# Kernel optimization log

Measured on AMD Instinct MI355X. Metric: run time of the kernel, lower is better.

The kernel has to match this reference:

```python
import jax, jax.numpy as jnp
import numpy as np

D_MODEL = 768
NUM_HEADS = 12
DEPTH = D_MODEL // NUM_HEADS
LN_EPS = 1e-5


def setup_inputs() -> dict:
    key = jax.random.key(0)
    ks = jax.random.split(key, 5)
    B, S = 2, 2048
    scale = 1.0 / np.sqrt(D_MODEL)
    return {
        "Q": jax.random.normal(ks[0], (B, S, D_MODEL), jnp.float32),
        "W_q": jax.random.normal(ks[1], (D_MODEL, D_MODEL), jnp.float32) * scale,
        "b_q": jnp.zeros((D_MODEL,), jnp.float32),
        "W_k": jax.random.normal(ks[2], (D_MODEL, D_MODEL), jnp.float32) * scale,
        "b_k": jnp.zeros((D_MODEL,), jnp.float32),
        "W_v": jax.random.normal(ks[3], (D_MODEL, D_MODEL), jnp.float32) * scale,
        "b_v": jnp.zeros((D_MODEL,), jnp.float32),
        "W_o": jax.random.normal(ks[4], (D_MODEL, D_MODEL), jnp.float32) * scale,
        "b_o": jnp.zeros((D_MODEL,), jnp.float32),
        "ln_gamma": jnp.ones((D_MODEL,), jnp.float32),
        "ln_beta": jnp.zeros((D_MODEL,), jnp.float32),
    }


def _split_heads(x, B):
    # [B, S, D] -> [B, H, S, depth]
    return x.reshape(B, -1, NUM_HEADS, DEPTH).transpose(0, 2, 1, 3)


def reference(Q, W_q, b_q, W_k, b_k, W_v, b_v, W_o, b_o, ln_gamma, ln_beta):
    B = Q.shape[0]
    residual = Q
    # torch Linear: x @ W.T + b
    q = _split_heads(Q @ W_q.T + b_q, B)  # [B,H,S,dh]
    k = _split_heads(Q @ W_k.T + b_k, B)
    v = _split_heads(Q @ W_v.T + b_v, B)
    scores = jnp.einsum("bhqd,bhkd->bhqk", q, k) / jnp.sqrt(jnp.float32(DEPTH))
    attn = jax.nn.softmax(scores, axis=-1)
    out = jnp.einsum("bhqk,bhkd->bhqd", attn, v)
    out = out.transpose(0, 2, 1, 3).reshape(B, -1, D_MODEL)
    out = out @ W_o.T + b_o
    x = out + residual
    mu = jnp.mean(x, axis=-1, keepdims=True)
    var = jnp.mean(jnp.square(x - mu), axis=-1, keepdims=True)
    return (x - mu) * jax.lax.rsqrt(var + LN_EPS) * ln_gamma + ln_beta
```

## Files before the change

kernel.cpp:

```cpp
#include <hip/hip_runtime.h>
#include <hip/hip_bf16.h>

#define D_MODEL 768
#define S_LEN   2048
#define BATCH   2
#define NHEAD   12
#define DH      64
#define NTOK    (BATCH * S_LEN)
#define NBH     (BATCH * NHEAD)

typedef __attribute__((ext_vector_type(8))) short bf16x8;
typedef __attribute__((ext_vector_type(4))) float f32x4;

__device__ inline unsigned short f2bf(float f) {
    union { float f; unsigned u; } v; v.f = f;
    unsigned u = v.u;
    u += 0x7fffu + ((u >> 16) & 1u);
    return (unsigned short)(u >> 16);
}

__device__ inline unsigned pack_bf2(float a, float b) {
    union { __hip_bfloat162 h2; unsigned u; } cv;
    cv.h2 = __float22bfloat162_rn(make_float2(a, b));
    return cv.u;
}

__device__ inline float bf2f(unsigned short u) {
    union { unsigned u; float f; } c; c.u = ((unsigned)u) << 16; return c.f;
}

__device__ inline void stage16(const void* g, void* l) {
    __builtin_amdgcn_global_load_lds(
        (const __attribute__((address_space(1))) unsigned*)g,
        (__attribute__((address_space(3))) unsigned*)l, 16, 0, 0);
}

__global__ __launch_bounds__(256) void convert_kernel(
    const float* __restrict__ Q,
    const float* __restrict__ Wq, const float* __restrict__ Wk,
    const float* __restrict__ Wv, const float* __restrict__ Wo,
    unsigned short* __restrict__ Xb,
    unsigned short* __restrict__ Wqb, unsigned short* __restrict__ Wkb,
    unsigned short* __restrict__ Wvb, unsigned short* __restrict__ Wob)
{
    const int XV = NTOK * D_MODEL / 4;
    const int WV = D_MODEL * D_MODEL / 4;
    int idx = blockIdx.x * 256 + threadIdx.x;
    if (idx >= XV + 4 * WV) return;

    const float* src; unsigned short* dst; int off;
    if (idx < XV) { src = Q; dst = Xb; off = idx; }
    else {
        int i2 = idx - XV;
        int seg = i2 / WV; off = i2 - seg * WV;
        if      (seg == 0) { src = Wq; dst = Wqb; }
        else if (seg == 1) { src = Wk; dst = Wkb; }
        else if (seg == 2) { src = Wv; dst = Wvb; }
        else               { src = Wo; dst = Wob; }
    }
    float4 v = reinterpret_cast<const float4*>(src)[off];
    uint2 o;
    o.x = pack_bf2(v.x, v.y);
    o.y = pack_bf2(v.z, v.w);
    reinterpret_cast<uint2*>(dst)[off] = o;
}

#define STAGE_TILE(glob, rowstrideB, row0, k0, ldsbase, nIss)                 \
    _Pragma("unroll")                                                          \
    for (int i = 0; i < (nIss); ++i) {                                         \
        int L = i * 4096 + wv * 1024 + lane * 16;                              \
        int row = L >> 7;                                                      \
        int colb = (L & 127) ^ ((row & 7) << 4);                               \
        stage16((const char*)(glob) + (size_t)((row0) + row) * (rowstrideB)    \
                    + ((k0) << 1) + colb,                                      \
                (char*)(ldsbase) + i * 4096 + wv * 1024);                      \
    }

__global__ __launch_bounds__(256) void qkv_gemm_kernel(
    const unsigned short* __restrict__ Xb,
    const unsigned short* __restrict__ Wall,
    const float* __restrict__ bq, const float* __restrict__ bk,
    const float* __restrict__ bv,
    unsigned short* __restrict__ qb, unsigned short* __restrict__ kb,
    unsigned short* __restrict__ vtb)
{
    const int lane = threadIdx.x & 63;
    const int wv   = threadIdx.x >> 6;
    const int lr   = lane & 15;
    const int lg   = lane >> 4;
    const int row0g = blockIdx.y * 128;
    const int col0g = blockIdx.x * 64;

    __shared__ __align__(16) unsigned short At[2][128 * 64];
    __shared__ __align__(16) unsigned short Bt[2][64 * 64];

    f32x4 acc[2][4] = {};

    STAGE_TILE(Xb,   1536, row0g, 0, At[0], 4);
    STAGE_TILE(Wall, 1536, col0g, 0, Bt[0], 2);
    __syncthreads();

    for (int s = 0; s < 12; ++s) {
        int cur = s & 1;
        if (s < 11) {
            STAGE_TILE(Xb,   1536, row0g, (s + 1) * 64, At[cur ^ 1], 4);
            STAGE_TILE(Wall, 1536, col0g, (s + 1) * 64, Bt[cur ^ 1], 2);
        }
        bf16x8 a[2][2], b[4][2];
#pragma unroll
        for (int m = 0; m < 2; ++m) {
            int row = wv * 32 + m * 16 + lr, sw = (row & 7) << 4;
#pragma unroll
            for (int ks = 0; ks < 2; ++ks)
                a[m][ks] = *reinterpret_cast<const bf16x8*>(
                    (const char*)At[cur] + row * 128 + ((ks * 64 + lg * 16) ^ sw));
        }
#pragma unroll
        for (int n = 0; n < 4; ++n) {
            int row = n * 16 + lr, sw = (row & 7) << 4;
#pragma unroll
            for (int ks = 0; ks < 2; ++ks)
                b[n][ks] = *reinterpret_cast<const bf16x8*>(
                    (const char*)Bt[cur] + row * 128 + ((ks * 64 + lg * 16) ^ sw));
        }
#pragma unroll
        for (int ks = 0; ks < 2; ++ks)
#pragma unroll
            for (int m = 0; m < 2; ++m)
#pragma unroll
                for (int n = 0; n < 4; ++n)
                    acc[m][n] = __builtin_amdgcn_mfma_f32_16x16x32_bf16(
                        a[m][ks], b[n][ks], acc[m][n], 0, 0, 0);
        __syncthreads();
    }

    const int which   = blockIdx.x / 12;
    const int colbase = (blockIdx.x % 12) * 64;
    const float* bias = (which == 0) ? bq : (which == 1) ? bk : bv;
#pragma unroll
    for (int m = 0; m < 2; ++m) {
#pragma unroll
        for (int n = 0; n < 4; ++n) {
            int col = colbase + n * 16 + lr;
            float bval = bias[col];
            int h = col >> 6, d = col & 63;
            int rowg = row0g + wv * 32 + m * 16 + lg * 4;
            int bb = rowg >> 11, s0 = rowg & 2047;
            if (which == 2) {
                uint2 w;
                w.x = pack_bf2(acc[m][n][0] + bval, acc[m][n][1] + bval);
                w.y = pack_bf2(acc[m][n][2] + bval, acc[m][n][3] + bval);
                *reinterpret_cast<uint2*>(
                    vtb + ((size_t)(bb * NHEAD + h) * DH + d) * S_LEN + s0) = w;
            } else {
                unsigned short* dst = (which == 0) ? qb : kb;
#pragma unroll
                for (int r = 0; r < 4; ++r)
                    dst[((size_t)(bb * NHEAD + h) * S_LEN + s0 + r) * DH + d] =
                        f2bf(acc[m][n][r] + bval);
            }
        }
    }
}

#define ATTN_CHUNK(P, CI, NCHUNK)                                              \
    {                                                                          \
        if ((CI) < (NCHUNK) - 1) {                                             \
            _Pragma("unroll")                                                  \
            for (int i = 0; i < SPW; ++i) {                                    \
                stage16(kg[i], sdK[(P) ^ 1] + i * 1024);                       \
                stage16(vg[i], sdV[(P) ^ 1] + i * 1024);                       \
                kg[i] += 8192; vg[i] += 128;                                   \
            }                                                                  \
        }                                                                      \
        f32x4 s[4] = {};                                                       \
        __builtin_amdgcn_s_setprio(1);                                         \
        _Pragma("unroll")                                                      \
        for (int kt = 0; kt < 4; ++kt) {                                       \
            bf16x8 ak0 = *(const bf16x8*)(rdK[P] + kt * 2048);                 \
            bf16x8 ak1 = *(const bf16x8*)(rdK[P] + kt * 2048 + oD);            \
            s[kt] = __builtin_amdgcn_mfma_f32_16x16x32_bf16(ak0, bq0, s[kt], 0, 0, 0); \
            s[kt] = __builtin_amdgcn_mfma_f32_16x16x32_bf16(ak1, bq1, s[kt], 0, 0, 0); \
        }                                                                      \
        __builtin_amdgcn_s_setprio(0);                                         \
        bf16x8 av0[4], av1[4];                                                 \
        _Pragma("unroll")                                                      \
        for (int t = 0; t < 4; ++t) {                                          \
            av0[t] = *(const bf16x8*)(rdV[P] + t * 2048);                      \
            av1[t] = *(const bf16x8*)(rdV[P] + t * 2048 + oD);                 \
        }                                                                      \
        float mxr = fmaxf(fmaxf(fmaxf(s[0][0], s[0][1]), fmaxf(s[0][2], s[0][3])), \
                          fmaxf(fmaxf(s[1][0], s[1][1]), fmaxf(s[1][2], s[1][3]))); \
        mxr = fmaxf(mxr, fmaxf(fmaxf(fmaxf(s[2][0], s[2][1]), fmaxf(s[2][2], s[2][3])), \
                               fmaxf(fmaxf(s[3][0], s[3][1]), fmaxf(s[3][2], s[3][3])))); \
        mxr = fmaxf(mxr, __shfl_xor(mxr, 16));                                 \
        mxr = fmaxf(mxr, __shfl_xor(mxr, 32));                                 \
        float mxs = mxr * SC;                                                  \
        if (__any(mxs > m + 8.0f)) {                                           \
            float mn = fmaxf(m, mxs);                                          \
            float sf = __builtin_amdgcn_exp2f(m - mn);                         \
            m = mn; l *= sf;                                                   \
            _Pragma("unroll")                                                  \
            for (int t = 0; t < 4; ++t) acc[t] *= sf;                          \
        }                                                                      \
        float p[16];                                                           \
        _Pragma("unroll")                                                      \
        for (int kt = 0; kt < 4; ++kt)                                         \
            _Pragma("unroll")                                                  \
            for (int r = 0; r < 4; ++r)                                        \
                p[kt * 4 + r] = __builtin_amdgcn_exp2f(fmaf(s[kt][r], SC, -m)); \
        float sum = ((p[0] + p[1]) + (p[2] + p[3])) + ((p[4] + p[5]) + (p[6] + p[7])); \
        sum += ((p[8] + p[9]) + (p[10] + p[11])) + ((p[12] + p[13]) + (p[14] + p[15])); \
        sum += __shfl_xor(sum, 16);                                            \
        sum += __shfl_xor(sum, 32);                                            \
        l += sum;                                                              \
        _Pragma("unroll")                                                      \
        for (int kt = 0; kt < 4; ++kt) {                                       \
            uint2 w;                                                           \
            w.x = pack_bf2(p[kt * 4 + 0], p[kt * 4 + 1]);                      \
            w.y = pack_bf2(p[kt * 4 + 2], p[kt * 4 + 3]);                      \
            *(uint2*)(plw + kt * 32 + lg * 8) = w;                             \
        }                                                                      \
        union { bf16x8 v; uint2 u[2]; } bp0, bp1;                              \
        bp0.u[0] = *(const uint2*)(plr);                                       \
        bp0.u[1] = *(const uint2*)(plr + 8);                                   \
        bp1.u[0] = *(const uint2*)(plr + 64);                                  \
        bp1.u[1] = *(const uint2*)(plr + 72);                                  \
        __builtin_amdgcn_s_setprio(1);                                         \
        _Pragma("unroll")                                                      \
        for (int t = 0; t < 4; ++t) {                                          \
            acc[t] = __builtin_amdgcn_mfma_f32_16x16x32_bf16(av0[t], bp0.v, acc[t], 0, 0, 0); \
            acc[t] = __builtin_amdgcn_mfma_f32_16x16x32_bf16(av1[t], bp1.v, acc[t], 0, 0, 0); \
        }                                                                      \
        __builtin_amdgcn_s_setprio(0);                                         \
        __syncthreads();                                                       \
    }

template<int NW, int KS>
__global__ __launch_bounds__(NW * 64) void attn_kernel(
    const unsigned short* __restrict__ qb, const unsigned short* __restrict__ kb,
    const unsigned short* __restrict__ vtb,
    unsigned short* __restrict__ attnb,
    unsigned short* __restrict__ Opart,
    float2* __restrict__ mlbuf)
{
    constexpr int SPW    = 8192 / (NW * 1024);
    constexpr int NCHUNK = 32 / KS;

    const int lane = threadIdx.x & 63;
    const int wv   = threadIdx.x >> 6;
    const int lr   = lane & 15;
    const int lg   = lane >> 4;
    const int bh   = blockIdx.y;
    const int h    = bh % NHEAD, bb = bh / NHEAD;
    const int q0   = blockIdx.x * (NW * 16) + wv * 16;
    const int ks   = (KS == 2) ? blockIdx.z : 0;

    __shared__ __align__(16) unsigned short Kt[2][4096];
    __shared__ __align__(16) unsigned short Vt[2][4096];
    __shared__ __align__(16) unsigned short PL[NW][16][68];

    const char* kbase = (const char*)(kb  + (size_t)bh * S_LEN * DH)
                        + (size_t)ks * (S_LEN / KS) * 128;
    const char* vbase = (const char*)(vtb + (size_t)bh * DH * S_LEN)
                        + (size_t)ks * (S_LEN / KS) * 2;
    const unsigned short* qptr = qb + ((size_t)bh * S_LEN + q0) * DH;

    bf16x8 bq0 = *reinterpret_cast<const bf16x8*>(qptr + (size_t)lr * DH + lg * 8);
    bf16x8 bq1 = *reinterpret_cast<const bf16x8*>(qptr + (size_t)lr * DH + 32 + lg * 8);

    const int swr = (lr & 7) << 4;
    const int o0  = (lg * 16) ^ swr;
    const int oD  = (o0 ^ 64) - o0;

    const char* kg[SPW];
    const char* vg[SPW];
#pragma unroll
    for (int i = 0; i < SPW; ++i) {
        int L = wv * SPW * 1024 + i * 1024 + lane * 16;
        int r = L >> 7;
        int c = (L & 127) ^ ((r & 7) << 4);
        kg[i] = kbase + (size_t)r * 128 + c;
        vg[i] = vbase + (size_t)r * 4096 + c;
    }
    char* sdK[2] = { (char*)Kt[0] + wv * SPW * 1024, (char*)Kt[1] + wv * SPW * 1024 };
    char* sdV[2] = { (char*)Vt[0] + wv * SPW * 1024, (char*)Vt[1] + wv * SPW * 1024 };
    const char* rdK[2] = {
        (const char*)Kt[0] + lr * 128 + o0,
        (const char*)Kt[1] + lr * 128 + o0 };
    const char* rdV[2] = {
        (const char*)Vt[0] + lr * 128 + o0,
        (const char*)Vt[1] + lr * 128 + o0 };
    char* plw = (char*)PL + wv * 2176 + lr * 136;
    const char* plr = plw + lg * 16;

    float m = -1e30f, l = 0.f;
    f32x4 acc[4] = {};
    const float SC = 0.125f * 1.44269504088896f;

#pragma unroll
    for (int i = 0; i < SPW; ++i) {
        stage16(kg[i], sdK[0] + i * 1024);
        stage16(vg[i], sdV[0] + i * 1024);
        kg[i] += 8192; vg[i] += 128;
    }
    __syncthreads();

    for (int it = 0; it < NCHUNK / 2; ++it) {
        ATTN_CHUNK(0, it * 2, NCHUNK);
        ATTN_CHUNK(1, it * 2 + 1, NCHUNK);
    }

    if constexpr (KS == 1) {
        float rl = 1.0f / l;
        size_t rowbase = ((size_t)(bb * S_LEN + q0 + lr)) * D_MODEL + h * DH;
#pragma unroll
        for (int t = 0; t < 4; ++t) {
            unsigned w0 = pack_bf2(acc[t][0] * rl, acc[t][1] * rl);
            unsigned w1 = pack_bf2(acc[t][2] * rl, acc[t][3] * rl);
            *reinterpret_cast<unsigned*>(attnb + rowbase + t * 16 + lg * 4)     = w0;
            *reinterpret_cast<unsigned*>(attnb + rowbase + t * 16 + lg * 4 + 2) = w1;
        }
    } else {
        size_t base = ((size_t)(ks * NBH + bh) * S_LEN + q0 + lr) * 64;
#pragma unroll
        for (int t = 0; t < 4; ++t) {
            unsigned w0 = pack_bf2(acc[t][0], acc[t][1]);
            unsigned w1 = pack_bf2(acc[t][2], acc[t][3]);
            *reinterpret_cast<unsigned*>(Opart + base + t * 16 + lg * 4)     = w0;
            *reinterpret_cast<unsigned*>(Opart + base + t * 16 + lg * 4 + 2) = w1;
        }
        if (lg == 0)
            mlbuf[(size_t)(ks * NBH + bh) * S_LEN + q0 + lr] = make_float2(m, l);
    }
}

__global__ __launch_bounds__(256) void combine_kernel(
    const unsigned short* __restrict__ Opart,
    const float2* __restrict__ mlbuf,
    unsigned short* __restrict__ attnb)
{
    int idx = blockIdx.x * 256 + threadIdx.x;
    int d4  = idx & 15;
    int h   = (idx >> 4) % 12;
    int tok = idx / 192;
    int bb  = tok >> 11, s = tok & 2047;
    size_t qoff = (size_t)(bb * NHEAD + h) * S_LEN + s;

    float2 ml0 = mlbuf[qoff];
    float2 ml1 = mlbuf[(size_t)NBH * S_LEN + qoff];
    float M  = fmaxf(ml0.x, ml1.x);
    float w0 = __builtin_amdgcn_exp2f(ml0.x - M);
    float w1 = __builtin_amdgcn_exp2f(ml1.x - M);
    float ri = 1.0f / (w0 * ml0.y + w1 * ml1.y);
    w0 *= ri; w1 *= ri;

    size_t ob = qoff * 64 + d4 * 4;
    ushort4 a = *reinterpret_cast<const ushort4*>(Opart + ob);
    ushort4 b = *reinterpret_cast<const ushort4*>(Opart + (size_t)NBH * S_LEN * 64 + ob);
    float o0 = bf2f(a.x) * w0 + bf2f(b.x) * w1;
    float o1 = bf2f(a.y) * w0 + bf2f(b.y) * w1;
    float o2 = bf2f(a.z) * w0 + bf2f(b.z) * w1;
    float o3 = bf2f(a.w) * w0 + bf2f(b.w) * w1;
    uint2 w;
    w.x = pack_bf2(o0, o1);
    w.y = pack_bf2(o2, o3);
    *reinterpret_cast<uint2*>(attnb + (size_t)tok * D_MODEL + h * 64 + d4 * 4) = w;
}

__global__ __launch_bounds__(256) void oproj_kernel(
    const unsigned short* __restrict__ attnb, const unsigned short* __restrict__ Wob,
    const float* __restrict__ bo, const float* __restrict__ Qres,
    float* __restrict__ Y)
{
    const int lane = threadIdx.x & 63;
    const int wv   = threadIdx.x >> 6;
    const int lr   = lane & 15;
    const int lg   = lane >> 4;
    const int row0g = blockIdx.y * 128;
    const int col0g = blockIdx.x * 64;

    __shared__ __align__(16) unsigned short At[2][128 * 64];
    __shared__ __align__(16) unsigned short Bt[2][64 * 64];

    f32x4 acc[2][4] = {};

    STAGE_TILE(attnb, 1536, row0g, 0, At[0], 4);
    STAGE_TILE(Wob,   1536, col0g, 0, Bt[0], 2);
    __syncthreads();

    for (int s = 0; s < 12; ++s) {
        int cur = s & 1;
        if (s < 11) {
            STAGE_TILE(attnb, 1536, row0g, (s + 1) * 64, At[cur ^ 1], 4);
            STAGE_TILE(Wob,   1536, col0g, (s + 1) * 64, Bt[cur ^ 1], 2);
        }
        bf16x8 a[2][2], b[4][2];
#pragma unroll
        for (int m = 0; m < 2; ++m) {
            int row = wv * 32 + m * 16 + lr, sw = (row & 7) << 4;
#pragma unroll
            for (int ks = 0; ks < 2; ++ks)
                a[m][ks] = *reinterpret_cast<const bf16x8*>(
                    (const char*)At[cur] + row * 128 + ((ks * 64 + lg * 16) ^ sw));
        }
#pragma unroll
        for (int n = 0; n < 4; ++n) {
            int row = n * 16 + lr, sw = (row & 7) << 4;
#pragma unroll
            for (int ks = 0; ks < 2; ++ks)
                b[n][ks] = *reinterpret_cast<const bf16x8*>(
                    (const char*)Bt[cur] + row * 128 + ((ks * 64 + lg * 16) ^ sw));
        }
#pragma unroll
        for (int ks = 0; ks < 2; ++ks)
#pragma unroll
            for (int m = 0; m < 2; ++m)
#pragma unroll
                for (int n = 0; n < 4; ++n)
                    acc[m][n] = __builtin_amdgcn_mfma_f32_16x16x32_bf16(
                        a[m][ks], b[n][ks], acc[m][n], 0, 0, 0);
        __syncthreads();
    }

#pragma unroll
    for (int m = 0; m < 2; ++m)
#pragma unroll
        for (int n = 0; n < 4; ++n) {
            int col = col0g + n * 16 + lr;
            float bval = bo[col];
#pragma unroll
            for (int r = 0; r < 4; ++r) {
                int row = row0g + wv * 32 + m * 16 + lg * 4 + r;
                size_t off = (size_t)row * D_MODEL + col;
                Y[off] = acc[m][n][r] + bval + Qres[off];
            }
        }
}

__global__ __launch_bounds__(256) void ln_kernel(
    const float* __restrict__ Y,
    const float* __restrict__ gamma, const float* __restrict__ beta,
    float* __restrict__ out)
{
    const int lane = threadIdx.x & 63;
    const int row  = blockIdx.x * 4 + (threadIdx.x >> 6);
    const float4* yr = reinterpret_cast<const float4*>(Y + (size_t)row * D_MODEL);

    float4 v[3];
    float sum = 0.f, ss = 0.f;
#pragma unroll
    for (int j = 0; j < 3; ++j) {
        v[j] = yr[lane + 64 * j];
        sum += v[j].x + v[j].y + v[j].z + v[j].w;
        ss  += v[j].x * v[j].x + v[j].y * v[j].y + v[j].z * v[j].z + v[j].w * v[j].w;
    }
#pragma unroll
    for (int msk = 1; msk < 64; msk <<= 1) {
        sum += __shfl_xor(sum, msk);
        ss  += __shfl_xor(ss,  msk);
    }
    float mu  = sum * (1.f / 768.f);
    float var = ss * (1.f / 768.f) - mu * mu;
    float is  = rsqrtf(var + 1e-5f);

    const float4* g4 = reinterpret_cast<const float4*>(gamma);
    const float4* b4 = reinterpret_cast<const float4*>(beta);
    float4* o4 = reinterpret_cast<float4*>(out + (size_t)row * D_MODEL);
#pragma unroll
    for (int j = 0; j < 3; ++j) {
        float4 g = g4[lane + 64 * j], b = b4[lane + 64 * j], r;
        r.x = (v[j].x - mu) * is * g.x + b.x;
        r.y = (v[j].y - mu) * is * g.y + b.y;
        r.z = (v[j].z - mu) * is * g.z + b.z;
        r.w = (v[j].w - mu) * is * g.w + b.w;
        o4[lane + 64 * j] = r;
    }
}

extern "C" void kernel_launch(void* const* d_in, const int* in_sizes, int n_in,
                              void* d_out, int out_size, void* d_ws, size_t ws_size,
                              hipStream_t stream)
{
    const float* Q     = (const float*)d_in[0];
    const float* Wq    = (const float*)d_in[1];
    const float* bq    = (const float*)d_in[2];
    const float* Wk    = (const float*)d_in[3];
    const float* bk    = (const float*)d_in[4];
    const float* Wv    = (const float*)d_in[5];
    const float* bv    = (const float*)d_in[6];
    const float* Wo    = (const float*)d_in[7];
    const float* bo    = (const float*)d_in[8];
    const float* gamma = (const float*)d_in[9];
    const float* beta  = (const float*)d_in[10];
    float* out = (float*)d_out;

    char* ws = (char*)d_ws;
    unsigned short* Xb    = (unsigned short*)(ws + 0);
    unsigned short* Wqb   = (unsigned short*)(ws + 6291456);
    unsigned short* Wkb   = (unsigned short*)(ws + 7471104);
    unsigned short* Wvb   = (unsigned short*)(ws + 8650752);
    unsigned short* Wob   = (unsigned short*)(ws + 9830400);
    unsigned short* qb    = (unsigned short*)(ws + 11010048);
    unsigned short* kb    = (unsigned short*)(ws + 17301504);
    unsigned short* vtb   = (unsigned short*)(ws + 23592960);
    unsigned short* attnb = (unsigned short*)(ws + 29884416);
    float*          Yf    = (float*)        (ws + 36175872);
    unsigned short* Opartb = (unsigned short*)(ws + 36175872);
    float2*         mlbuf  = (float2*)       (ws + 61341696);

    const bool splitk = (ws_size >= 62128128ull);

    convert_kernel<<<5376, 256, 0, stream>>>(Q, Wq, Wk, Wv, Wo, Xb, Wqb, Wkb, Wvb, Wob);
    qkv_gemm_kernel<<<dim3(36, 32), 256, 0, stream>>>(Xb, Wqb, bq, bk, bv, qb, kb, vtb);
    if (splitk) {
        attn_kernel<8, 2><<<dim3(16, 24, 2), 512, 0, stream>>>(qb, kb, vtb, attnb,
                                                               Opartb, mlbuf);
        combine_kernel<<<3072, 256, 0, stream>>>(Opartb, mlbuf, attnb);
    } else {
        attn_kernel<4, 1><<<dim3(32, 24), 256, 0, stream>>>(qb, kb, vtb, attnb,
                                                            Opartb, mlbuf);
    }
    oproj_kernel<<<dim3(12, 32), 256, 0, stream>>>(attnb, Wob, bo, Q, Yf);
    ln_kernel<<<1024, 256, 0, stream>>>(Yf, gamma, beta, out);
}
```

Baseline: 111.4 us.

## Triple-buffer K in attention, read V directly from global, enlarge QKV GEMM tiles

The QKV GEMM tile goes from 128x64 to 128x128, with a 2x2 warp layout and four by four accumulators per warp, so each block reuses its X tile across twice as many output columns. The attention kernel now triple-buffers only K in LDS, using explicit vmcnt waits and raw barriers instead of __syncthreads. V fragments are loaded straight from global memory per lane, and the cross-lane sum reductions and the max shuffles are deferred or moved inside the rare rescale branch. The non-split path moves to 512-thread blocks. This aims to cut LDS traffic, barrier stalls and shuffle work, at the cost of uncoalesced direct V global loads and more register pressure in the GEMM.

```diff
diff --git a/kernel.cpp b/kernel.cpp
--- a/kernel.cpp
+++ b/kernel.cpp
@@ -88,36 +88,38 @@
     const int wv   = threadIdx.x >> 6;
     const int lr   = lane & 15;
     const int lg   = lane >> 4;
+    const int wr   = wv >> 1;
+    const int wc   = wv & 1;
     const int row0g = blockIdx.y * 128;
-    const int col0g = blockIdx.x * 64;
+    const int col0g = blockIdx.x * 128;
 
     __shared__ __align__(16) unsigned short At[2][128 * 64];
-    __shared__ __align__(16) unsigned short Bt[2][64 * 64];
-
-    f32x4 acc[2][4] = {};
+    __shared__ __align__(16) unsigned short Bt[2][128 * 64];
+
+    f32x4 acc[4][4] = {};
 
     STAGE_TILE(Xb,   1536, row0g, 0, At[0], 4);
-    STAGE_TILE(Wall, 1536, col0g, 0, Bt[0], 2);
+    STAGE_TILE(Wall, 1536, col0g, 0, Bt[0], 4);
     __syncthreads();
 
     for (int s = 0; s < 12; ++s) {
         int cur = s & 1;
         if (s < 11) {
             STAGE_TILE(Xb,   1536, row0g, (s + 1) * 64, At[cur ^ 1], 4);
-            STAGE_TILE(Wall, 1536, col0g, (s + 1) * 64, Bt[cur ^ 1], 2);
-        }
-        bf16x8 a[2][2], b[4][2];
-#pragma unroll
-        for (int m = 0; m < 2; ++m) {
-            int row = wv * 32 + m * 16 + lr, sw = (row & 7) << 4;
+            STAGE_TILE(Wall, 1536, col0g, (s + 1) * 64, Bt[cur ^ 1], 4);
+        }
+        bf16x8 a[4][2], b[4][2];
+#pragma unroll
+        for (int mm = 0; mm < 4; ++mm) {
+            int row = wr * 64 + mm * 16 + lr, sw = (row & 7) << 4;
 #pragma unroll
             for (int ks = 0; ks < 2; ++ks)
-                a[m][ks] = *reinterpret_cast<const bf16x8*>(
+                a[mm][ks] = *reinterpret_cast<const bf16x8*>(
                     (const char*)At[cur] + row * 128 + ((ks * 64 + lg * 16) ^ sw));
         }
 #pragma unroll
         for (int n = 0; n < 4; ++n) {
-            int row = n * 16 + lr, sw = (row & 7) << 4;
+            int row = wc * 64 + n * 16 + lr, sw = (row & 7) << 4;
 #pragma unroll
             for (int ks = 0; ks < 2; ++ks)
                 b[n][ks] = *reinterpret_cast<const bf16x8*>(
@@ -126,30 +128,30 @@
 #pragma unroll
         for (int ks = 0; ks < 2; ++ks)
 #pragma unroll
-            for (int m = 0; m < 2; ++m)
+            for (int mm = 0; mm < 4; ++mm)
 #pragma unroll
                 for (int n = 0; n < 4; ++n)
-                    acc[m][n] = __builtin_amdgcn_mfma_f32_16x16x32_bf16(
-                        a[m][ks], b[n][ks], acc[m][n], 0, 0, 0);
+                    acc[mm][n] = __builtin_amdgcn_mfma_f32_16x16x32_bf16(
+                        a[mm][ks], b[n][ks], acc[mm][n], 0, 0, 0);
         __syncthreads();
     }
 
-    const int which   = blockIdx.x / 12;
-    const int colbase = (blockIdx.x % 12) * 64;
+    const int which   = blockIdx.x / 6;
+    const int colbase = (blockIdx.x % 6) * 128;
     const float* bias = (which == 0) ? bq : (which == 1) ? bk : bv;
 #pragma unroll
-    for (int m = 0; m < 2; ++m) {
+    for (int mm = 0; mm < 4; ++mm) {
 #pragma unroll
         for (int n = 0; n < 4; ++n) {
-            int col = colbase + n * 16 + lr;
+            int col = colbase + wc * 64 + n * 16 + lr;
             float bval = bias[col];
             int h = col >> 6, d = col & 63;
-            int rowg = row0g + wv * 32 + m * 16 + lg * 4;
+            int rowg = row0g + wr * 64 + mm * 16 + lg * 4;
             int bb = rowg >> 11, s0 = rowg & 2047;
             if (which == 2) {
                 uint2 w;
-                w.x = pack_bf2(acc[m][n][0] + bval, acc[m][n][1] + bval);
-                w.y = pack_bf2(acc[m][n][2] + bval, acc[m][n][3] + bval);
+                w.x = pack_bf2(acc[mm][n][0] + bval, acc[mm][n][1] + bval);
+                w.y = pack_bf2(acc[mm][n][2] + bval, acc[mm][n][3] + bval);
                 *reinterpret_cast<uint2*>(
                     vtb + ((size_t)(bb * NHEAD + h) * DH + d) * S_LEN + s0) = w;
             } else {
@@ -157,22 +159,22 @@
 #pragma unroll
                 for (int r = 0; r < 4; ++r)
                     dst[((size_t)(bb * NHEAD + h) * S_LEN + s0 + r) * DH + d] =
-                        f2bf(acc[m][n][r] + bval);
+                        f2bf(acc[mm][n][r] + bval);
             }
         }
     }
 }
 
-#define ATTN_CHUNK(P, CI, NCHUNK)                                              \
+#define AC(P, NXT, DOSTAGE, WN, DOBAR)                                         \
     {                                                                          \
-        if ((CI) < (NCHUNK) - 1) {                                             \
-            _Pragma("unroll")                                                  \
-            for (int i = 0; i < SPW; ++i) {                                    \
-                stage16(kg[i], sdK[(P) ^ 1] + i * 1024);                       \
-                stage16(vg[i], sdV[(P) ^ 1] + i * 1024);                       \
-                kg[i] += 8192; vg[i] += 128;                                   \
-            }                                                                  \
+        bf16x8 av0[4], av1[4];                                                 \
+        _Pragma("unroll")                                                      \
+        for (int t = 0; t < 4; ++t) {                                          \
+            av0[t] = *(const bf16x8*)(vp[t]);                                  \
+            av1[t] = *(const bf16x8*)(vp[t] + 64);                             \
+            vp[t] += 128;                                                      \
         }                                                                      \
+        if (DOSTAGE) { stage16(kg, sdK[NXT]); kg += 8192; }                    \
         f32x4 s[4] = {};                                                       \
         __builtin_amdgcn_s_setprio(1);                                         \
         _Pragma("unroll")                                                      \
@@ -183,21 +185,17 @@
             s[kt] = __builtin_amdgcn_mfma_f32_16x16x32_bf16(ak1, bq1, s[kt], 0, 0, 0); \
         }                                                                      \
         __builtin_amdgcn_s_setprio(0);                                         \
-        bf16x8 av0[4], av1[4];                                                 \
-        _Pragma("unroll")                                                      \
-        for (int t = 0; t < 4; ++t) {                                          \
-            av0[t] = *(const bf16x8*)(rdV[P] + t * 2048);                      \
-            av1[t] = *(const bf16x8*)(rdV[P] + t * 2048 + oD);                 \
-        }                                                                      \
-        float mxr = fmaxf(fmaxf(fmaxf(s[0][0], s[0][1]), fmaxf(s[0][2], s[0][3])), \
-                          fmaxf(fmaxf(s[1][0], s[1][1]), fmaxf(s[1][2], s[1][3]))); \
-        mxr = fmaxf(mxr, fmaxf(fmaxf(fmaxf(s[2][0], s[2][1]), fmaxf(s[2][2], s[2][3])), \
-                               fmaxf(fmaxf(s[3][0], s[3][1]), fmaxf(s[3][2], s[3][3])))); \
-        mxr = fmaxf(mxr, __shfl_xor(mxr, 16));                                 \
-        mxr = fmaxf(mxr, __shfl_xor(mxr, 32));                                 \
-        float mxs = mxr * SC;                                                  \
-        if (__any(mxs > m + 8.0f)) {                                           \
-            float mn = fmaxf(m, mxs);                                          \
+        float g0 = fmaxf(fmaxf(s[0][0], s[0][1]), s[0][2]);                    \
+        float g1 = fmaxf(fmaxf(s[0][3], s[1][0]), s[1][1]);                    \
+        float g2 = fmaxf(fmaxf(s[1][2], s[1][3]), s[2][0]);                    \
+        float g3 = fmaxf(fmaxf(s[2][1], s[2][2]), s[2][3]);                    \
+        float g4 = fmaxf(fmaxf(s[3][0], s[3][1]), s[3][2]);                    \
+        float mx = fmaxf(fmaxf(fmaxf(g0, g1), g2), fmaxf(fmaxf(g3, g4), s[3][3])); \
+        if (__any(mx * SC > m + 8.0f)) {                                       \
+            float mg = mx * SC;                                                \
+            mg = fmaxf(mg, __shfl_xor(mg, 16));                                \
+            mg = fmaxf(mg, __shfl_xor(mg, 32));                                \
+            float mn = fmaxf(m, mg);                                           \
             float sf = __builtin_amdgcn_exp2f(m - mn);                         \
             m = mn; l *= sf;                                                   \
             _Pragma("unroll")                                                  \
@@ -211,8 +209,6 @@
                 p[kt * 4 + r] = __builtin_amdgcn_exp2f(fmaf(s[kt][r], SC, -m)); \
         float sum = ((p[0] + p[1]) + (p[2] + p[3])) + ((p[4] + p[5]) + (p[6] + p[7])); \
         sum += ((p[8] + p[9]) + (p[10] + p[11])) + ((p[12] + p[13]) + (p[14] + p[15])); \
-        sum += __shfl_xor(sum, 16);                                            \
-        sum += __shfl_xor(sum, 32);                                            \
         l += sum;                                                              \
         _Pragma("unroll")                                                      \
         for (int kt = 0; kt < 4; ++kt) {                                       \
@@ -233,32 +229,32 @@
             acc[t] = __builtin_amdgcn_mfma_f32_16x16x32_bf16(av1[t], bp1.v, acc[t], 0, 0, 0); \
         }                                                                      \
         __builtin_amdgcn_s_setprio(0);                                         \
-        __syncthreads();                                                       \
-    }
-
-template<int NW, int KS>
-__global__ __launch_bounds__(NW * 64) void attn_kernel(
+        if (DOBAR) {                                                           \
+            if (WN) asm volatile("s_waitcnt vmcnt(1)");                        \
+            else    asm volatile("s_waitcnt vmcnt(0)");                        \
+            __builtin_amdgcn_s_barrier();                                      \
+        }                                                                      \
+    }
+
+template<int KS>
+__global__ __launch_bounds__(512) void attn_kernel(
     const unsigned short* __restrict__ qb, const unsigned short* __restrict__ kb,
     const unsigned short* __restrict__ vtb,
     unsigned short* __restrict__ attnb,
     unsigned short* __restrict__ Opart,
     float2* __restrict__ mlbuf)
 {
-    constexpr int SPW    = 8192 / (NW * 1024);
-    constexpr int NCHUNK = 32 / KS;
-
     const int lane = threadIdx.x & 63;
     const int wv   = threadIdx.x >> 6;
     const int lr   = lane & 15;
     const int lg   = lane >> 4;
     const int bh   = blockIdx.y;
     const int h    = bh % NHEAD, bb = bh / NHEAD;
-    const int q0   = blockIdx.x * (NW * 16) + wv * 16;
+    const int q0   = blockIdx.x * 128 + wv * 16;
     const int ks   = (KS == 2) ? blockIdx.z : 0;
 
-    __shared__ __align__(16) unsigned short Kt[2][4096];
-    __shared__ __align__(16) unsigned short Vt[2][4096];
-    __shared__ __align__(16) unsigned short PL[NW][16][68];
+    __shared__ __align__(16) unsigned short Kt[3][4096];
+    __shared__ __align__(16) unsigned short PL[8][16][68];
 
     const char* kbase = (const char*)(kb  + (size_t)bh * S_LEN * DH)
                         + (size_t)ks * (S_LEN / KS) * 128;
@@ -272,44 +268,52 @@
     const int swr = (lr & 7) << 4;
     const int o0  = (lg * 16) ^ swr;
     const int oD  = (o0 ^ 64) - o0;
-
-    const char* kg[SPW];
-    const char* vg[SPW];
-#pragma unroll
-    for (int i = 0; i < SPW; ++i) {
-        int L = wv * SPW * 1024 + i * 1024 + lane * 16;
-        int r = L >> 7;
-        int c = (L & 127) ^ ((r & 7) << 4);
-        kg[i] = kbase + (size_t)r * 128 + c;
-        vg[i] = vbase + (size_t)r * 4096 + c;
-    }
-    char* sdK[2] = { (char*)Kt[0] + wv * SPW * 1024, (char*)Kt[1] + wv * SPW * 1024 };
-    char* sdV[2] = { (char*)Vt[0] + wv * SPW * 1024, (char*)Vt[1] + wv * SPW * 1024 };
-    const char* rdK[2] = {
+    const int L1  = wv * 1024 + lane * 16;
+    const int r1  = L1 >> 7;
+    const int cb1 = (L1 & 127) ^ ((r1 & 7) << 4);
+
+    const char* kg = kbase + (size_t)r1 * 128 + cb1;
+    char* sdK[3] = { (char*)Kt[0] + wv * 1024, (char*)Kt[1] + wv * 1024,
+                     (char*)Kt[2] + wv * 1024 };
+    const char* rdK[3] = {
         (const char*)Kt[0] + lr * 128 + o0,
-        (const char*)Kt[1] + lr * 128 + o0 };
-    const char* rdV[2] = {
-        (const char*)Vt[0] + lr * 128 + o0,
-        (const char*)Vt[1] + lr * 128 + o0 };
+        (const char*)Kt[1] + lr * 128 + o0,
+        (const char*)Kt[2] + lr * 128 + o0 };
     char* plw = (char*)PL + wv * 2176 + lr * 136;
     const char* plr = plw + lg * 16;
+
+    const char* vp[4];
+#pragma unroll
+    for (int t = 0; t < 4; ++t)
+        vp[t] = vbase + (size_t)(t * 16 + lr) * 4096 + lg * 16;
 
     float m = -1e30f, l = 0.f;
     f32x4 acc[4] = {};
     const float SC = 0.125f * 1.44269504088896f;
 
-#pragma unroll
-    for (int i = 0; i < SPW; ++i) {
-        stage16(kg[i], sdK[0] + i * 1024);
-        stage16(vg[i], sdV[0] + i * 1024);
-        kg[i] += 8192; vg[i] += 128;
-    }
-    __syncthreads();
-
-    for (int it = 0; it < NCHUNK / 2; ++it) {
-        ATTN_CHUNK(0, it * 2, NCHUNK);
-        ATTN_CHUNK(1, it * 2 + 1, NCHUNK);
-    }
+    stage16(kg, sdK[0]); kg += 8192;
+    stage16(kg, sdK[1]); kg += 8192;
+    asm volatile("s_waitcnt vmcnt(1)");
+    __builtin_amdgcn_s_barrier();
+
+    if constexpr (KS == 2) {
+        for (int it = 0; it < 4; ++it) {
+            AC(0, 2, 1, 1, 1); AC(1, 0, 1, 1, 1); AC(2, 1, 1, 1, 1);
+        }
+        AC(0, 2, 1, 1, 1);
+        AC(1, 0, 1, 1, 1);
+        AC(2, 1, 0, 0, 1);
+        AC(0, 2, 0, 0, 0);
+    } else {
+        for (int it = 0; it < 10; ++it) {
+            AC(0, 2, 1, 1, 1); AC(1, 0, 1, 1, 1); AC(2, 1, 1, 1, 1);
+        }
+        AC(0, 2, 0, 0, 1);
+        AC(1, 0, 0, 0, 0);
+    }
+
+    l += __shfl_xor(l, 16);
+    l += __shfl_xor(l, 32);
 
     if constexpr (KS == 1) {
         float rl = 1.0f / l;
@@ -397,11 +401,11 @@
         }
         bf16x8 a[2][2], b[4][2];
 #pragma unroll
-        for (int m = 0; m < 2; ++m) {
-            int row = wv * 32 + m * 16 + lr, sw = (row & 7) << 4;
+        for (int mm = 0; mm < 2; ++mm) {
+            int row = wv * 32 + mm * 16 + lr, sw = (row & 7) << 4;
 #pragma unroll
             for (int ks = 0; ks < 2; ++ks)
-                a[m][ks] = *reinterpret_cast<const bf16x8*>(
+                a[mm][ks] = *reinterpret_cast<const bf16x8*>(
                     (const char*)At[cur] + row * 128 + ((ks * 64 + lg * 16) ^ sw));
         }
 #pragma unroll
@@ -415,25 +419,25 @@
 #pragma unroll
         for (int ks = 0; ks < 2; ++ks)
 #pragma unroll
-            for (int m = 0; m < 2; ++m)
+            for (int mm = 0; mm < 2; ++mm)
 #pragma unroll
                 for (int n = 0; n < 4; ++n)
-                    acc[m][n] = __builtin_amdgcn_mfma_f32_16x16x32_bf16(
-                        a[m][ks], b[n][ks], acc[m][n], 0, 0, 0);
+                    acc[mm][n] = __builtin_amdgcn_mfma_f32_16x16x32_bf16(
+                        a[mm][ks], b[n][ks], acc[mm][n], 0, 0, 0);
         __syncthreads();
     }
 
 #pragma unroll
-    for (int m = 0; m < 2; ++m)
+    for (int mm = 0; mm < 2; ++mm)
 #pragma unroll
         for (int n = 0; n < 4; ++n) {
             int col = col0g + n * 16 + lr;
             float bval = bo[col];
 #pragma unroll
             for (int r = 0; r < 4; ++r) {
-                int row = row0g + wv * 32 + m * 16 + lg * 4 + r;
+                int row = row0g + wv * 32 + mm * 16 + lg * 4 + r;
                 size_t off = (size_t)row * D_MODEL + col;
-                Y[off] = acc[m][n][r] + bval + Qres[off];
+                Y[off] = acc[mm][n][r] + bval + Qres[off];
             }
         }
 }
@@ -512,14 +516,14 @@
     const bool splitk = (ws_size >= 62128128ull);
 
     convert_kernel<<<5376, 256, 0, stream>>>(Q, Wq, Wk, Wv, Wo, Xb, Wqb, Wkb, Wvb, Wob);
-    qkv_gemm_kernel<<<dim3(36, 32), 256, 0, stream>>>(Xb, Wqb, bq, bk, bv, qb, kb, vtb);
+    qkv_gemm_kernel<<<dim3(18, 32), 256, 0, stream>>>(Xb, Wqb, bq, bk, bv, qb, kb, vtb);
     if (splitk) {
-        attn_kernel<8, 2><<<dim3(16, 24, 2), 512, 0, stream>>>(qb, kb, vtb, attnb,
-                                                               Opartb, mlbuf);
+        attn_kernel<2><<<dim3(16, 24, 2), 512, 0, stream>>>(qb, kb, vtb, attnb,
+                                                            Opartb, mlbuf);
         combine_kernel<<<3072, 256, 0, stream>>>(Opartb, mlbuf, attnb);
     } else {
-        attn_kernel<4, 1><<<dim3(32, 24), 256, 0, stream>>>(qb, kb, vtb, attnb,
-                                                            Opartb, mlbuf);
+        attn_kernel<1><<<dim3(16, 24), 512, 0, stream>>>(qb, kb, vtb, attnb,
+                                                         Opartb, mlbuf);
     }
     oproj_kernel<<<dim3(12, 32), 256, 0, stream>>>(attnb, Wob, bo, Q, Yf);
     ln_kernel<<<1024, 256, 0, stream>>>(Yf, gamma, beta, out);
```

Measured after the change: 169.7 us. 1.52x slower.
